# Kernel optimization log

Measured on AMD Instinct MI355X. Metric: run time of the kernel, lower is better.

## Reference

```python
import jax, jax.numpy as jnp
import numpy as np

EPS = 0.1        # entropic regularization (init eps)
MAX_ITER = 100   # init max_iter
THRESH = 0.1     # early-stop threshold from original code
NORM_EPS = 1e-8


def setup_inputs() -> dict:
    key = jax.random.key(0)
    kx, ky = jax.random.split(key)
    x = jax.random.normal(kx, (16, 1024, 256), dtype=jnp.float32)
    y = jax.random.normal(ky, (16, 1024, 256), dtype=jnp.float32)
    return {"x": x, "y": y}


def _mfa_cost(x, y):
    # Cosine cost: E = 1 - cos(x_i, y_j), computed via normalized matmul
    # (norms clamped at 1e-8 as in torch CosineSimilarity).
    xn = x / jnp.maximum(jnp.linalg.norm(x, axis=-1, keepdims=True), NORM_EPS)
    yn = y / jnp.maximum(jnp.linalg.norm(y, axis=-1, keepdims=True), NORM_EPS)
    E = 1.0 - jnp.einsum('bnd,bmd->bnm', xn, yn)  # [B, N, M]

    B, N, M = E.shape
    log_mu = jnp.full((B, N), jnp.log(1.0 / N + 1e-8), dtype=E.dtype)
    log_nu = jnp.full((B, M), jnp.log(1.0 / M + 1e-8), dtype=E.dtype)

    def Mmat(u, v):
        # (-E + u_i + v_j) / eps, broadcast over [B, N, M]
        return (-E + u[..., :, None] + v[..., None, :]) / EPS

    @jax.checkpoint
    def body(carry, _):
        u, v, done = carry
        u_new = EPS * (log_mu - jax.nn.logsumexp(Mmat(u, v), axis=-1)) + u
        # original transposes then logsumexp over -1 == logsumexp over -2
        v_new = EPS * (log_nu - jax.nn.logsumexp(Mmat(u_new, v), axis=-2)) + v
        err = jnp.abs(u_new - u).sum(-1).mean()
        # emulate data-dependent break: freeze u, v once converged
        u_out = jnp.where(done, u, u_new)
        v_out = jnp.where(done, v, v_new)
        return (u_out, v_out, done | (err < THRESH)), None

    u0 = jnp.zeros((B, N), dtype=E.dtype)
    v0 = jnp.zeros((B, M), dtype=E.dtype)
    (u, v, _), _ = jax.lax.scan(body, (u0, v0, jnp.array(False)), None, length=MAX_ITER)

    pi = jnp.exp(Mmat(u, v))                 # transport plan [B, N, M]
    cost = jnp.sum(pi * E, axis=(-2, -1))    # [B]  (reduction='none')
    return cost


def reference(x, y):
    return _mfa_cost(x, y)
```

## Files before the change

kernel.cpp:

```cpp
#include <hip/hip_runtime.h>

typedef _Float16 half_t;
typedef __attribute__((ext_vector_type(8))) _Float16 half8;
typedef __attribute__((ext_vector_type(4))) float f32x4;
typedef __attribute__((ext_vector_type(8))) short short8v;
typedef unsigned short u16;
typedef unsigned int u32;

#define SCALE_F     14.4269504f
#define INV_SCALE_F 0.0693147181f
#define C_MU       -9.99998523f
#define C_NU       -9.99998523f
#define MU_F        0.000976572498f
#define ERR_STOP_B  1.44269504f
#define MAX_ITER    100
#define SPIN_LIMIT  50000000LL

#define SMEM_E   131072
#define SMEM_CP  16384
#define SMEM_V   4096
#define SMEM_RED 256
#define SMEM_TOTAL (SMEM_E + SMEM_CP + SMEM_V + SMEM_RED)

#define PSTRIDE  1040
#define PWORDS   (2*16*16*PSTRIDE)

__device__ __forceinline__ float fexp2(float x) { return __builtin_amdgcn_exp2f(x); }
__device__ __forceinline__ float flog2(float x) { return __builtin_amdgcn_logf(x); }
__device__ __forceinline__ float frcp(float x)  { return __builtin_amdgcn_rcpf(x); }

__device__ __forceinline__ u16 f2bf(float f) {
  unsigned u = __float_as_uint(f);
  return (u16)((u + 0x7fffu + ((u >> 16) & 1u)) >> 16);
}

__device__ __forceinline__ u32 agload(const u32* p) {
  return __hip_atomic_load(p, __ATOMIC_RELAXED, __HIP_MEMORY_SCOPE_AGENT);
}
__device__ __forceinline__ void agstore(u32* p, u32 v) {
  __hip_atomic_store(p, v, __ATOMIC_RELAXED, __HIP_MEMORY_SCOPE_AGENT);
}

__global__ __launch_bounds__(256) void mfa_prep(const float* __restrict__ x,
                                                const float* __restrict__ y,
                                                u16* __restrict__ Xn,
                                                u16* __restrict__ Yn,
                                                u32* __restrict__ partials,
                                                float* __restrict__ cost) {
  int g = blockIdx.x * 256 + threadIdx.x;
  if (g < 16) cost[g] = 0.0f;
  #pragma unroll
  for (int j = 0; j < 9; ++j) {
    int idx = (j << 16) + g;
    if (idx < PWORDS) partials[idx] = 0u;
  }

  int wid = g >> 6;
  int lane = threadIdx.x & 63;
  for (int rr = 0; rr < 32; ++rr) {
    int row = wid + (rr << 10);
    const float* src = (row < 16384) ? x + (size_t)row * 256
                                     : y + (size_t)(row - 16384) * 256;
    float4 xa = ((const float4*)src)[lane];
    float ss = xa.x*xa.x + xa.y*xa.y + xa.z*xa.z + xa.w*xa.w;
    #pragma unroll
    for (int off = 32; off; off >>= 1) ss += __shfl_xor(ss, off);
    float inv = 1.0f / fmaxf(sqrtf(ss), 1e-8f);
    ushort4 o;
    o.x = f2bf(xa.x * inv); o.y = f2bf(xa.y * inv);
    o.z = f2bf(xa.z * inv); o.w = f2bf(xa.w * inv);
    u16* dst = ((row < 16384) ? Xn + ((size_t)row << 8)
                              : Yn + ((size_t)(row - 16384) << 8)) + lane * 4;
    *(ushort4*)dst = o;
  }
}

__global__ __launch_bounds__(512, 1) void mfa_sink_fused(
    const u16* __restrict__ Xn, const u16* __restrict__ Yn,
    u32* __restrict__ partials, float* __restrict__ cost) {
  extern __shared__ char smem[];
  half_t* Els  = (half_t*)smem;
  float*  cpb  = (float*)(smem + SMEM_E);
  float*  vsh  = (float*)(smem + SMEM_E + SMEM_CP);
  float*  sred = (float*)(smem + SMEM_E + SMEM_CP + SMEM_V);

  const int t = threadIdx.x, w = t >> 6, lane = t & 63;
  const int lane15 = lane & 15, lgrp = lane >> 4;
  const int blk = blockIdx.x;
  const int b = ((blk & 7) << 1) | ((blk >> 7) & 1);
  const int k = (blk >> 3) & 15;

  {
    const u16* Xb = Xn + ((size_t)((b << 10) + (k << 6)) << 8);
    const u16* Yb = Yn + ((size_t)(b << 10) << 8);
    const int wcol = w << 7;
    #pragma unroll
    for (int pass = 0; pass < 2; ++pass) {
      const int c0 = wcol + (pass << 6);
      f32x4 acc[4][4];
      #pragma unroll
      for (int i = 0; i < 4; ++i)
        #pragma unroll
        for (int j = 0; j < 4; ++j) acc[i][j] = (f32x4){0.f, 0.f, 0.f, 0.f};
      for (int ks = 0; ks < 8; ++ks) {
        const int koff = (ks << 5) + (lgrp << 3);
        short8v a[4], bb[4];
        #pragma unroll
        for (int i = 0; i < 4; ++i)
          a[i] = *(const short8v*)(Xb + (((i << 4) + lane15) << 8) + koff);
        #pragma unroll
        for (int j = 0; j < 4; ++j)
          bb[j] = *(const short8v*)(Yb + ((size_t)(c0 + (j << 4) + lane15) << 8) + koff);
        #pragma unroll
        for (int i = 0; i < 4; ++i)
          #pragma unroll
          for (int j = 0; j < 4; ++j)
            acc[i][j] = __builtin_amdgcn_mfma_f32_16x16x32_bf16(a[i], bb[j], acc[i][j], 0, 0, 0);
      }
      #pragma unroll
      for (int i = 0; i < 4; ++i)
        #pragma unroll
        for (int j = 0; j < 4; ++j) {
          const int col = c0 + (j << 4) + lane15;
          #pragma unroll
          for (int q = 0; q < 4; ++q) {
            const int row = (i << 4) + (lgrp << 2) + q;
            Els[(row << 10) + col] = (half_t)((1.0f - acc[i][j][q]) * SCALE_F);
          }
        }
    }
  }
  vsh[t] = 0.0f; vsh[t + 512] = 0.0f;
  __syncthreads();

  float ureg[8];
  #pragma unroll
  for (int r = 0; r < 8; ++r) ureg[r] = 0.0f;

  const int mlo = lane << 3;
  int it = 0;
  for (; it < MAX_ITER; ++it) {
    const f32x4* v4 = (const f32x4*)vsh;
    f32x4 va4 = v4[lane*2], vb4 = v4[lane*2 + 1];
    f32x4 vc4 = v4[128 + lane*2], vd4 = v4[128 + lane*2 + 1];
    float vv[16];
    vv[0]=va4.x; vv[1]=va4.y; vv[2]=va4.z; vv[3]=va4.w;
    vv[4]=vb4.x; vv[5]=vb4.y; vv[6]=vb4.z; vv[7]=vb4.w;
    vv[8]=vc4.x; vv[9]=vc4.y; vv[10]=vc4.z; vv[11]=vc4.w;
    vv[12]=vd4.x; vv[13]=vd4.y; vv[14]=vd4.z; vv[15]=vd4.w;

    float colacc[16];
    #pragma unroll
    for (int j = 0; j < 16; ++j) colacc[j] = 0.0f;
    float werr = 0.0f;

    #pragma unroll
    for (int r = 0; r < 8; ++r) {
      const half8* E8 = (const half8*)(Els + (((w << 3) + r) << 10));
      half8 ea = E8[lane], eb = E8[lane + 64];
      float rt[16];
      float s = 0.0f;
      #pragma unroll
      for (int j = 0; j < 8; ++j) { rt[j] = fexp2(vv[j] - (float)ea[j]); s += rt[j]; }
      #pragma unroll
      for (int j = 0; j < 8; ++j) { rt[8+j] = fexp2(vv[8+j] - (float)eb[j]); s += rt[8+j]; }
      #pragma unroll
      for (int off = 32; off; off >>= 1) s += __shfl_xor(s, off);
      float unew = C_MU - flog2(s);
      float eu = MU_F * frcp(s);
      werr += fabsf(unew - ureg[r]);
      ureg[r] = unew;
      #pragma unroll
      for (int j = 0; j < 16; ++j) colacc[j] += rt[j] * eu;
    }
    if (lane == 0) sred[w] = werr;

    if (w < 4) {
      #pragma unroll
      for (int j = 0; j < 4; ++j) {
        *(f32x4*)&cpb[w*1024 + mlo + 4*j - ((j>=2)?8:0) + ((j>=2)?512:0)] =
            (f32x4){colacc[4*j], colacc[4*j+1], colacc[4*j+2], colacc[4*j+3]};
      }
    }
    __syncthreads();
    if (w >= 4) {
      const int wb = (w - 4) * 1024;
      #pragma unroll
      for (int j = 0; j < 8; ++j) cpb[wb + mlo + j] += colacc[j];
      #pragma unroll
      for (int j = 0; j < 8; ++j) cpb[wb + 512 + mlo + j] += colacc[8 + j];
    }
    __syncthreads();

    const int p = it & 1;
    const u32 tag = (u32)((it + 1) & 3);
    {
      u32* ps = partials + (size_t)((((p << 4) | b) << 4) | k) * PSTRIDE;
      float2 q0 = *(const float2*)&cpb[2*t];
      float2 q1 = *(const float2*)&cpb[1024 + 2*t];
      float2 q2 = *(const float2*)&cpb[2048 + 2*t];
      float2 q3 = *(const float2*)&cpb[3072 + 2*t];
      float ca = q0.x + q1.x + q2.x + q3.x;
      float cb = q0.y + q1.y + q2.y + q3.y;
      agstore(&ps[2*t],     (__float_as_uint(ca) & ~3u) | tag);
      agstore(&ps[2*t + 1], (__float_as_uint(cb) & ~3u) | tag);
      if (t == 0) {
        float be = sred[0]+sred[1]+sred[2]+sred[3]+sred[4]+sred[5]+sred[6]+sred[7];
        agstore(&ps[1024], (__float_as_uint(be) & ~3u) | tag);
      }
    }

    {
      const u32* pb32 = partials + (size_t)(((p << 4) | b) << 4) * PSTRIDE;
      u32 wa[16], wb[16];
      #pragma unroll
      for (int j = 0; j < 16; ++j) {
        wa[j] = agload(&pb32[j * PSTRIDE + 2*t]);
        wb[j] = agload(&pb32[j * PSTRIDE + 2*t + 1]);
      }
      long long tws = clock64();
      #pragma unroll
      for (int j = 0; j < 16; ++j) {
        while ((wa[j] & 3u) != tag) {
          wa[j] = agload(&pb32[j * PSTRIDE + 2*t]);
          if (clock64() - tws > SPIN_LIMIT) break;
        }
        while ((wb[j] & 3u) != tag) {
          wb[j] = agload(&pb32[j * PSTRIDE + 2*t + 1]);
          if (clock64() - tws > SPIN_LIMIT) break;
        }
      }
      float t0s = 0.0f, t1s = 0.0f;
      #pragma unroll
      for (int j = 0; j < 16; ++j) {
        t0s += __uint_as_float(wa[j]);
        t1s += __uint_as_float(wb[j]);
      }
      if (w == 0) {
        float we = 0.0f;
        if (lane < 16) {
          u32 ww = agload(&pb32[lane * PSTRIDE + 1024]);
          while ((ww & 3u) != tag) {
            ww = agload(&pb32[lane * PSTRIDE + 1024]);
            if (clock64() - tws > SPIN_LIMIT) break;
          }
          we = __uint_as_float(ww);
        }
        #pragma unroll
        for (int off = 8; off; off >>= 1) we += __shfl_xor(we, off);
        if (lane == 0) sred[8] = we;
      }
      vsh[2*t]     += C_NU - flog2(t0s);
      vsh[2*t + 1] += C_NU - flog2(t1s);
    }
    __syncthreads();

    if (sred[8] < ERR_STOP_B) break;
  }

  {
    const f32x4* v4 = (const f32x4*)vsh;
    f32x4 va4 = v4[lane*2], vb4 = v4[lane*2 + 1];
    f32x4 vc4 = v4[128 + lane*2], vd4 = v4[128 + lane*2 + 1];
    float vv[16];
    vv[0]=va4.x; vv[1]=va4.y; vv[2]=va4.z; vv[3]=va4.w;
    vv[4]=vb4.x; vv[5]=vb4.y; vv[6]=vb4.z; vv[7]=vb4.w;
    vv[8]=vc4.x; vv[9]=vc4.y; vv[10]=vc4.z; vv[11]=vc4.w;
    vv[12]=vd4.x; vv[13]=vd4.y; vv[14]=vd4.z; vv[15]=vd4.w;
    float cacc = 0.0f;
    #pragma unroll
    for (int r = 0; r < 8; ++r) {
      const half8* E8 = (const half8*)(Els + (((w << 3) + r) << 10));
      half8 ea = E8[lane], eb = E8[lane + 64];
      float un = ureg[r];
      #pragma unroll
      for (int j = 0; j < 8; ++j) {
        float e = (float)ea[j];
        cacc += fexp2(un + vv[j] - e) * e;
      }
      #pragma unroll
      for (int j = 0; j < 8; ++j) {
        float e = (float)eb[j];
        cacc += fexp2(un + vv[8+j] - e) * e;
      }
    }
    #pragma unroll
    for (int off = 32; off; off >>= 1) cacc += __shfl_xor(cacc, off);
    if (lane == 0) sred[w] = cacc;
    __syncthreads();
    if (t == 0)
      atomicAdd(&cost[b], (sred[0]+sred[1]+sred[2]+sred[3]+sred[4]+sred[5]+
                           sred[6]+sred[7]) * INV_SCALE_F);
  }
}

extern "C" void kernel_launch(void* const* d_in, const int* in_sizes, int n_in,
                              void* d_out, int out_size, void* d_ws, size_t ws_size,
                              hipStream_t stream) {
  const float* x = (const float*)d_in[0];
  const float* y = (const float*)d_in[1];
  float* cost = (float*)d_out;

  char* base = (char*)d_ws;
  u16* Xn       = (u16*)base;
  u16* Yn       = (u16*)(base + 8388608);
  u32* partials = (u32*)(base + 16777216);
  size_t needed = 16777216 + (size_t)PWORDS * 4;
  if (ws_size < needed) return;

  mfa_prep<<<256, 256, 0, stream>>>(x, y, Xn, Yn, partials, cost);

  (void)hipFuncSetAttribute((const void*)mfa_sink_fused,
                            hipFuncAttributeMaxDynamicSharedMemorySize, SMEM_TOTAL);
  mfa_sink_fused<<<dim3(256), dim3(512), SMEM_TOTAL, stream>>>(
      Xn, Yn, partials, cost);
}
```

Before: 83.02 us.

## Store exp(-E) kernel in LDS and replace per-iteration exps with FMAs; bf16 partials with flag sync

The cost matrix is now kept in LDS as the scaled kernel exp2(15 - E/eps), and v as exp2(v - 15). Each Sinkhorn row sum therefore becomes an FMA dot product instead of 16 exp2 evaluations per row per iteration. Cross-block column partials are packed as two bf16 values per word, with separate per-wave flags and sleep-polling replacing the per-word tag spinning. This removes the transcendental bottleneck and halves global exchange traffic. In exchange it risks fp16 underflow or overflow of the kernel values, bf16 precision loss in the partial sums, and less accurate cost recovery via log2.

```diff
diff --git a/kernel.cpp b/kernel.cpp
--- a/kernel.cpp
+++ b/kernel.cpp
@@ -15,15 +15,16 @@
 #define ERR_STOP_B  1.44269504f
 #define MAX_ITER    100
 #define SPIN_LIMIT  50000000LL
+#define PV0         3.0517578125e-05f
 
 #define SMEM_E   131072
 #define SMEM_CP  16384
-#define SMEM_V   4096
+#define SMEM_PV  4096
 #define SMEM_RED 256
-#define SMEM_TOTAL (SMEM_E + SMEM_CP + SMEM_V + SMEM_RED)
-
-#define PSTRIDE  1040
-#define PWORDS   (2*16*16*PSTRIDE)
+#define SMEM_TOTAL (SMEM_E + SMEM_CP + SMEM_PV + SMEM_RED)
+
+#define PSTRIDE  520
+#define NFLAGS   2048
 
 __device__ __forceinline__ float fexp2(float x) { return __builtin_amdgcn_exp2f(x); }
 __device__ __forceinline__ float flog2(float x) { return __builtin_amdgcn_logf(x); }
@@ -33,11 +34,19 @@
   unsigned u = __float_as_uint(f);
   return (u16)((u + 0x7fffu + ((u >> 16) & 1u)) >> 16);
 }
-
+__device__ __forceinline__ float bf2f(u16 h) {
+  return __uint_as_float(((unsigned)h) << 16);
+}
 __device__ __forceinline__ u32 agload(const u32* p) {
   return __hip_atomic_load(p, __ATOMIC_RELAXED, __HIP_MEMORY_SCOPE_AGENT);
 }
 __device__ __forceinline__ void agstore(u32* p, u32 v) {
+  __hip_atomic_store(p, v, __ATOMIC_RELAXED, __HIP_MEMORY_SCOPE_AGENT);
+}
+__device__ __forceinline__ int agload_i(const int* p) {
+  return __hip_atomic_load(p, __ATOMIC_RELAXED, __HIP_MEMORY_SCOPE_AGENT);
+}
+__device__ __forceinline__ void agstore_i(int* p, int v) {
   __hip_atomic_store(p, v, __ATOMIC_RELAXED, __HIP_MEMORY_SCOPE_AGENT);
 }
 
@@ -45,15 +54,11 @@
                                                 const float* __restrict__ y,
                                                 u16* __restrict__ Xn,
                                                 u16* __restrict__ Yn,
-                                                u32* __restrict__ partials,
+                                                int* __restrict__ flags,
                                                 float* __restrict__ cost) {
   int g = blockIdx.x * 256 + threadIdx.x;
+  if (g < NFLAGS) flags[g] = 0;
   if (g < 16) cost[g] = 0.0f;
-  #pragma unroll
-  for (int j = 0; j < 9; ++j) {
-    int idx = (j << 16) + g;
-    if (idx < PWORDS) partials[idx] = 0u;
-  }
 
   int wid = g >> 6;
   int lane = threadIdx.x & 63;
@@ -77,18 +82,20 @@
 
 __global__ __launch_bounds__(512, 1) void mfa_sink_fused(
     const u16* __restrict__ Xn, const u16* __restrict__ Yn,
-    u32* __restrict__ partials, float* __restrict__ cost) {
+    u32* __restrict__ partials, int* __restrict__ flags,
+    float* __restrict__ cost) {
   extern __shared__ char smem[];
-  half_t* Els  = (half_t*)smem;
+  half_t* pEls = (half_t*)smem;
   float*  cpb  = (float*)(smem + SMEM_E);
-  float*  vsh  = (float*)(smem + SMEM_E + SMEM_CP);
-  float*  sred = (float*)(smem + SMEM_E + SMEM_CP + SMEM_V);
+  float*  pvsh = (float*)(smem + SMEM_E + SMEM_CP);
+  float*  sred = (float*)(smem + SMEM_E + SMEM_CP + SMEM_PV);
 
   const int t = threadIdx.x, w = t >> 6, lane = t & 63;
   const int lane15 = lane & 15, lgrp = lane >> 4;
   const int blk = blockIdx.x;
   const int b = ((blk & 7) << 1) | ((blk >> 7) & 1);
   const int k = (blk >> 3) & 15;
+  const int idx = (w << 6) + lane;
 
   {
     const u16* Xb = Xn + ((size_t)((b << 10) + (k << 6)) << 8);
@@ -125,45 +132,49 @@
           #pragma unroll
           for (int q = 0; q < 4; ++q) {
             const int row = (i << 4) + (lgrp << 2) + q;
-            Els[(row << 10) + col] = (half_t)((1.0f - acc[i][j][q]) * SCALE_F);
+            pEls[(row << 10) + col] =
+                (half_t)fexp2(15.0f - (1.0f - acc[i][j][q]) * SCALE_F);
           }
         }
     }
   }
-  vsh[t] = 0.0f; vsh[t + 512] = 0.0f;
+  pvsh[t] = PV0; pvsh[t + 512] = PV0;
   __syncthreads();
 
   float ureg[8];
   #pragma unroll
   for (int r = 0; r < 8; ++r) ureg[r] = 0.0f;
+  float vr0 = 0.0f, vr1 = 0.0f;
 
   const int mlo = lane << 3;
   int it = 0;
   for (; it < MAX_ITER; ++it) {
-    const f32x4* v4 = (const f32x4*)vsh;
-    f32x4 va4 = v4[lane*2], vb4 = v4[lane*2 + 1];
-    f32x4 vc4 = v4[128 + lane*2], vd4 = v4[128 + lane*2 + 1];
-    float vv[16];
-    vv[0]=va4.x; vv[1]=va4.y; vv[2]=va4.z; vv[3]=va4.w;
-    vv[4]=vb4.x; vv[5]=vb4.y; vv[6]=vb4.z; vv[7]=vb4.w;
-    vv[8]=vc4.x; vv[9]=vc4.y; vv[10]=vc4.z; vv[11]=vc4.w;
-    vv[12]=vd4.x; vv[13]=vd4.y; vv[14]=vd4.z; vv[15]=vd4.w;
-
-    float colacc[16];
-    #pragma unroll
-    for (int j = 0; j < 16; ++j) colacc[j] = 0.0f;
+    const f32x4* p4 = (const f32x4*)pvsh;
+    f32x4 a4 = p4[lane*2], b4 = p4[lane*2 + 1];
+    f32x4 c4 = p4[128 + lane*2], d4 = p4[128 + lane*2 + 1];
+    float pv[16];
+    pv[0]=a4.x; pv[1]=a4.y; pv[2]=a4.z; pv[3]=a4.w;
+    pv[4]=b4.x; pv[5]=b4.y; pv[6]=b4.z; pv[7]=b4.w;
+    pv[8]=c4.x; pv[9]=c4.y; pv[10]=c4.z; pv[11]=c4.w;
+    pv[12]=d4.x; pv[13]=d4.y; pv[14]=d4.z; pv[15]=d4.w;
+
+    float inner[16];
+    #pragma unroll
+    for (int j = 0; j < 16; ++j) inner[j] = 0.0f;
     float werr = 0.0f;
 
     #pragma unroll
     for (int r = 0; r < 8; ++r) {
-      const half8* E8 = (const half8*)(Els + (((w << 3) + r) << 10));
+      const half8* E8 = (const half8*)(pEls + (((w << 3) + r) << 10));
       half8 ea = E8[lane], eb = E8[lane + 64];
-      float rt[16];
+      float pe[16];
+      #pragma unroll
+      for (int j = 0; j < 8; ++j) pe[j] = (float)ea[j];
+      #pragma unroll
+      for (int j = 0; j < 8; ++j) pe[8 + j] = (float)eb[j];
       float s = 0.0f;
       #pragma unroll
-      for (int j = 0; j < 8; ++j) { rt[j] = fexp2(vv[j] - (float)ea[j]); s += rt[j]; }
-      #pragma unroll
-      for (int j = 0; j < 8; ++j) { rt[8+j] = fexp2(vv[8+j] - (float)eb[j]); s += rt[8+j]; }
+      for (int j = 0; j < 16; ++j) s = __builtin_fmaf(pv[j], pe[j], s);
       #pragma unroll
       for (int off = 32; off; off >>= 1) s += __shfl_xor(s, off);
       float unew = C_MU - flog2(s);
@@ -171,8 +182,11 @@
       werr += fabsf(unew - ureg[r]);
       ureg[r] = unew;
       #pragma unroll
-      for (int j = 0; j < 16; ++j) colacc[j] += rt[j] * eu;
-    }
+      for (int j = 0; j < 16; ++j) inner[j] = __builtin_fmaf(pe[j], eu, inner[j]);
+    }
+    float colacc[16];
+    #pragma unroll
+    for (int j = 0; j < 16; ++j) colacc[j] = inner[j] * pv[j];
     if (lane == 0) sred[w] = werr;
 
     if (w < 4) {
@@ -193,65 +207,63 @@
     __syncthreads();
 
     const int p = it & 1;
-    const u32 tag = (u32)((it + 1) & 3);
+    u32* ps = partials + (size_t)((((p << 4) | b) << 4) | k) * PSTRIDE;
     {
-      u32* ps = partials + (size_t)((((p << 4) | b) << 4) | k) * PSTRIDE;
-      float2 q0 = *(const float2*)&cpb[2*t];
-      float2 q1 = *(const float2*)&cpb[1024 + 2*t];
-      float2 q2 = *(const float2*)&cpb[2048 + 2*t];
-      float2 q3 = *(const float2*)&cpb[3072 + 2*t];
-      float ca = q0.x + q1.x + q2.x + q3.x;
-      float cb = q0.y + q1.y + q2.y + q3.y;
-      agstore(&ps[2*t],     (__float_as_uint(ca) & ~3u) | tag);
-      agstore(&ps[2*t + 1], (__float_as_uint(cb) & ~3u) | tag);
+      const int c0 = idx << 1;
+      float2 q0 = *(const float2*)&cpb[c0];
+      float2 q1 = *(const float2*)&cpb[1024 + c0];
+      float2 q2 = *(const float2*)&cpb[2048 + c0];
+      float2 q3 = *(const float2*)&cpb[3072 + c0];
+      float fa  = q0.x + q1.x + q2.x + q3.x;
+      float fbv = q0.y + q1.y + q2.y + q3.y;
+      agstore(&ps[idx], (u32)f2bf(fa) | ((u32)f2bf(fbv) << 16));
       if (t == 0) {
         float be = sred[0]+sred[1]+sred[2]+sred[3]+sred[4]+sred[5]+sred[6]+sred[7];
-        agstore(&ps[1024], (__float_as_uint(be) & ~3u) | tag);
-      }
-    }
+        agstore(&ps[512], __float_as_uint(be));
+      }
+    }
+    asm volatile("s_waitcnt vmcnt(0)" ::: "memory");
+    if (lane == 0)
+      agstore_i(&flags[(b << 7) | (k << 3) | w], it + 1);
 
     {
-      const u32* pb32 = partials + (size_t)(((p << 4) | b) << 4) * PSTRIDE;
-      u32 wa[16], wb[16];
+      const int* fl = flags + (b << 7);
+      const int tgt = it + 1;
+      long long t0c = clock64();
+      for (;;) {
+        int f0 = agload_i(&fl[lane]);
+        int f1 = agload_i(&fl[lane + 64]);
+        if (__all((f0 >= tgt) && (f1 >= tgt))) break;
+        if (clock64() - t0c > SPIN_LIMIT) break;
+        __builtin_amdgcn_s_sleep(1);
+      }
+    }
+
+    {
+      const u32* pr = partials + (size_t)(((p << 4) | b) << 4) * PSTRIDE;
+      u32 wv[16];
+      #pragma unroll
+      for (int j = 0; j < 16; ++j)
+        wv[j] = agload(&pr[j * PSTRIDE + idx]);
+      float t0s = 0.0f, t1s = 0.0f;
       #pragma unroll
       for (int j = 0; j < 16; ++j) {
-        wa[j] = agload(&pb32[j * PSTRIDE + 2*t]);
-        wb[j] = agload(&pb32[j * PSTRIDE + 2*t + 1]);
-      }
-      long long tws = clock64();
-      #pragma unroll
-      for (int j = 0; j < 16; ++j) {
-        while ((wa[j] & 3u) != tag) {
-          wa[j] = agload(&pb32[j * PSTRIDE + 2*t]);
-          if (clock64() - tws > SPIN_LIMIT) break;
-        }
-        while ((wb[j] & 3u) != tag) {
-          wb[j] = agload(&pb32[j * PSTRIDE + 2*t + 1]);
-          if (clock64() - tws > SPIN_LIMIT) break;
-        }
-      }
-      float t0s = 0.0f, t1s = 0.0f;
-      #pragma unroll
-      for (int j = 0; j < 16; ++j) {
-        t0s += __uint_as_float(wa[j]);
-        t1s += __uint_as_float(wb[j]);
+        t0s += bf2f((u16)(wv[j] & 0xffffu));
+        t1s += bf2f((u16)(wv[j] >> 16));
       }
       if (w == 0) {
         float we = 0.0f;
-        if (lane < 16) {
-          u32 ww = agload(&pb32[lane * PSTRIDE + 1024]);
-          while ((ww & 3u) != tag) {
-            ww = agload(&pb32[lane * PSTRIDE + 1024]);
-            if (clock64() - tws > SPIN_LIMIT) break;
-          }
-          we = __uint_as_float(ww);
-        }
+        if (lane < 16)
+          we = __uint_as_float(agload(&pr[lane * PSTRIDE + 512]));
         #pragma unroll
         for (int off = 8; off; off >>= 1) we += __shfl_xor(we, off);
         if (lane == 0) sred[8] = we;
       }
-      vsh[2*t]     += C_NU - flog2(t0s);
-      vsh[2*t + 1] += C_NU - flog2(t1s);
+      const int c0 = idx << 1;
+      vr0 += C_NU - flog2(t0s);
+      vr1 += C_NU - flog2(t1s);
+      pvsh[c0]     = fexp2(vr0 - 15.0f);
+      pvsh[c0 + 1] = fexp2(vr1 - 15.0f);
     }
     __syncthreads();
 
@@ -259,29 +271,31 @@
   }
 
   {
-    const f32x4* v4 = (const f32x4*)vsh;
-    f32x4 va4 = v4[lane*2], vb4 = v4[lane*2 + 1];
-    f32x4 vc4 = v4[128 + lane*2], vd4 = v4[128 + lane*2 + 1];
-    float vv[16];
-    vv[0]=va4.x; vv[1]=va4.y; vv[2]=va4.z; vv[3]=va4.w;
-    vv[4]=vb4.x; vv[5]=vb4.y; vv[6]=vb4.z; vv[7]=vb4.w;
-    vv[8]=vc4.x; vv[9]=vc4.y; vv[10]=vc4.z; vv[11]=vc4.w;
-    vv[12]=vd4.x; vv[13]=vd4.y; vv[14]=vd4.z; vv[15]=vd4.w;
+    const f32x4* p4 = (const f32x4*)pvsh;
+    f32x4 a4 = p4[lane*2], b4 = p4[lane*2 + 1];
+    f32x4 c4 = p4[128 + lane*2], d4 = p4[128 + lane*2 + 1];
+    float pv[16];
+    pv[0]=a4.x; pv[1]=a4.y; pv[2]=a4.z; pv[3]=a4.w;
+    pv[4]=b4.x; pv[5]=b4.y; pv[6]=b4.z; pv[7]=b4.w;
+    pv[8]=c4.x; pv[9]=c4.y; pv[10]=c4.z; pv[11]=c4.w;
+    pv[12]=d4.x; pv[13]=d4.y; pv[14]=d4.z; pv[15]=d4.w;
     float cacc = 0.0f;
     #pragma unroll
     for (int r = 0; r < 8; ++r) {
-      const half8* E8 = (const half8*)(Els + (((w << 3) + r) << 10));
+      const half8* E8 = (const half8*)(pEls + (((w << 3) + r) << 10));
       half8 ea = E8[lane], eb = E8[lane + 64];
-      float un = ureg[r];
+      float su = fexp2(ureg[r]);
       #pragma unroll
       for (int j = 0; j < 8; ++j) {
-        float e = (float)ea[j];
-        cacc += fexp2(un + vv[j] - e) * e;
+        float pe = (float)ea[j];
+        float e = 15.0f - flog2(pe);
+        cacc += su * pv[j] * pe * e;
       }
       #pragma unroll
       for (int j = 0; j < 8; ++j) {
-        float e = (float)eb[j];
-        cacc += fexp2(un + vv[8+j] - e) * e;
+        float pe = (float)eb[j];
+        float e = 15.0f - flog2(pe);
+        cacc += su * pv[8 + j] * pe * e;
       }
     }
     #pragma unroll
@@ -305,13 +319,14 @@
   u16* Xn       = (u16*)base;
   u16* Yn       = (u16*)(base + 8388608);
   u32* partials = (u32*)(base + 16777216);
-  size_t needed = 16777216 + (size_t)PWORDS * 4;
+  int* flags    = (int*)(base + 16777216 + (size_t)2*16*16*PSTRIDE*4);
+  size_t needed = 16777216 + (size_t)2*16*16*PSTRIDE*4 + NFLAGS*4;
   if (ws_size < needed) return;
 
-  mfa_prep<<<256, 256, 0, stream>>>(x, y, Xn, Yn, partials, cost);
+  mfa_prep<<<256, 256, 0, stream>>>(x, y, Xn, Yn, flags, cost);
 
   (void)hipFuncSetAttribute((const void*)mfa_sink_fused,
                             hipFuncAttributeMaxDynamicSharedMemorySize, SMEM_TOTAL);
   mfa_sink_fused<<<dim3(256), dim3(512), SMEM_TOTAL, stream>>>(
-      Xn, Yn, partials, cost);
-}
+      Xn, Yn, partials, flags, cost);
+}
```

Measured after the change: 87.19 us. 1.05x slower.
